# Optimization experiments

Measured on AMD Instinct MI355X. Metric: run time of the kernel, lower is better.

## Reference

```python
import jax, jax.numpy as jnp
import numpy as np

N = 50000      # nodes / stations
E = 600000     # edges
IN = 16        # in_channels
ED = 8         # edge_dim
HID = 128      # hidden
H = 4          # heads
C = HID // H   # 32 per-head channels
EMB = HID // 2 # station embedding dim
FEAT = HID - EMB
SLOPE = 0.2    # GATv2 LeakyReLU negative slope


def setup_inputs() -> dict:
    key = jax.random.key(0)
    ks = jax.random.split(key, 32)
    r = lambda i, shape, s=0.05: (jax.random.normal(ks[i], shape, jnp.float32) * s)
    inp = {
        "x": jax.random.normal(ks[0], (N, IN), jnp.float32),
        "node_idx": jax.random.randint(ks[1], (N,), 0, N),
        "edge_index": jax.random.randint(ks[2], (2, E), 0, N),
        "edge_attr": jax.random.normal(ks[3], (E, ED), jnp.float32),
        # params
        "emb": r(4, (N, EMB)),
        "W_in": r(5, (IN, FEAT)), "b_in": jnp.zeros((FEAT,), jnp.float32),
        # conv1 (GATv2: lin_l, lin_r, lin_edge, att, out bias)
        "Wl1": r(6, (HID, HID)), "bl1": jnp.zeros((HID,), jnp.float32),
        "Wr1": r(7, (HID, HID)), "br1": jnp.zeros((HID,), jnp.float32),
        "We1": r(8, (ED, HID)),  "be1": jnp.zeros((HID,), jnp.float32),
        "att1": r(9, (H, C)),    "bo1": jnp.zeros((HID,), jnp.float32),
        # conv2
        "Wl2": r(10, (HID, HID)), "bl2": jnp.zeros((HID,), jnp.float32),
        "Wr2": r(11, (HID, HID)), "br2": jnp.zeros((HID,), jnp.float32),
        "We2": r(12, (ED, HID)),  "be2": jnp.zeros((HID,), jnp.float32),
        "att2": r(13, (H, C)),    "bo2": jnp.zeros((HID,), jnp.float32),
        # layer norms
        "g1": jnp.ones((HID,), jnp.float32), "beta1": jnp.zeros((HID,), jnp.float32),
        "g2": jnp.ones((HID,), jnp.float32), "beta2": jnp.zeros((HID,), jnp.float32),
        # output head
        "W_out": r(14, (HID, 1)), "b_out": jnp.zeros((1,), jnp.float32),
    }
    return inp


def _gatv2(x, src, dst, ea, Wl, bl, Wr, br, We, be, att, bo):
    # x: [N,HID] -> per-head projections [N,H,C]
    xl = (x @ Wl + bl).reshape(-1, H, C)   # source transform
    xr = (x @ Wr + br).reshape(-1, H, C)   # target transform
    ee = (ea @ We + be).reshape(-1, H, C)  # edge transform [E,H,C]
    s = jax.nn.leaky_relu(xl[src] + xr[dst] + ee, SLOPE)  # [E,H,C]
    logit = jnp.einsum('ehc,hc->eh', s, att)              # [E,H]
    # segment softmax over destination node
    amax = jax.lax.stop_gradient(jax.ops.segment_max(logit, dst, num_segments=N))
    amax = jnp.where(jnp.isfinite(amax), amax, 0.0)
    ex = jnp.exp(logit - amax[dst])
    den = jax.ops.segment_sum(ex, dst, num_segments=N)
    alpha = ex / den[dst]                                  # [E,H]
    out = jax.ops.segment_sum(xl[src] * alpha[..., None], dst, num_segments=N)
    return out.reshape(-1, HID) + bo


def _ln(x, g, b):
    mu = x.mean(-1, keepdims=True)
    v = ((x - mu) ** 2).mean(-1, keepdims=True)
    return (x - mu) * jax.lax.rsqrt(v + 1e-5) * g + b


def reference(x, node_idx, edge_index, edge_attr, emb, W_in, b_in,
              Wl1, bl1, Wr1, br1, We1, be1, att1, bo1,
              Wl2, bl2, Wr2, br2, We2, be2, att2, bo2,
              g1, beta1, g2, beta2, W_out, b_out):
    src, dst = edge_index[0], edge_index[1]
    feat = jax.nn.relu(x @ W_in + b_in)                       # [N,FEAT]
    z = jnp.concatenate([feat, emb[node_idx]], axis=-1)       # [N,HID]
    h = jax.nn.relu(_gatv2(z, src, dst, edge_attr, Wl1, bl1, Wr1, br1, We1, be1, att1, bo1))
    z = _ln(z + h, g1, beta1)
    h = jax.nn.relu(_gatv2(z, src, dst, edge_attr, Wl2, bl2, Wr2, br2, We2, be2, att2, bo2))
    z = _ln(z + h, g2, beta2)
    return (z @ W_out + b_out).squeeze(-1)                    # [N]
```

## Files before the change

### kernel.cpp

```cpp
#include <hip/hip_runtime.h>
#include <hip/hip_bf16.h>

#define NN 50000
#define NE 600000
#define IND 16
#define EDD 8
#define HIDD 128
#define NH 4
#define CC 32
#define EMBD 64
#define FEATD 64
#define NB_SCAN ((NN + 255) / 256)

typedef __hip_bfloat16 bf16;
typedef __attribute__((ext_vector_type(8))) short bshort8;
typedef __attribute__((ext_vector_type(4))) float floatx4;

__device__ __forceinline__ unsigned short f2bu(float f) {
    unsigned int u = __float_as_uint(f);
    u += 0x7fffu + ((u >> 16) & 1u);
    return (unsigned short)(u >> 16);
}

template <bool F32>
__device__ __forceinline__ float LD(const void* p, long long i) {
    if constexpr (F32) return ((const float*)p)[i];
    else return __bfloat162float(((const bf16*)p)[i]);
}

__device__ __forceinline__ bool is_f32(const int* cnt) { return *cnt > 8; }

__global__ void k_detinit(const unsigned short* __restrict__ x, int nhalf,
                          int* __restrict__ cnt, int* __restrict__ deg,
                          int* __restrict__ dcnt) {
    if (blockIdx.x == 0) {
        __shared__ int red[256];
        int hits = 0;
        for (int i = threadIdx.x; i < nhalf; i += 256)
            if ((x[i] & 0x7F80u) == 0x7F80u) hits++;
        red[threadIdx.x] = hits;
        __syncthreads();
        for (int o = 128; o; o >>= 1) {
            if (threadIdx.x < o) red[threadIdx.x] += red[threadIdx.x + o];
            __syncthreads();
        }
        if (threadIdx.x == 0) *cnt = red[0];
    } else {
        int gid = (blockIdx.x - 1) * 256 + threadIdx.x;
        if (gid < NN) deg[gid] = 0;
        if (blockIdx.x == 1 && threadIdx.x < 64) dcnt[threadIdx.x] = 0;
    }
}

__global__ void k_hist(const int* __restrict__ ei, int* __restrict__ deg, int* __restrict__ rank) {
    int e = blockIdx.x * blockDim.x + threadIdx.x;
    if (e < NE) rank[e] = atomicAdd(&deg[ei[NE + e]], 1);
}

__global__ void k_scan1(const int* __restrict__ deg, int* __restrict__ off,
                        int* __restrict__ bsum, int* __restrict__ dcnt,
                        int* __restrict__ rankd) {
    __shared__ int tile[256];
    __shared__ int lh[64];
    __shared__ int lbase[64];
    int t = threadIdx.x;
    int gid = blockIdx.x * 256 + t;
    if (t < 64) lh[t] = 0;
    __syncthreads();
    int v = (gid < NN) ? deg[gid] : 0;
    int b = min(v, 63);
    int lr = 0;
    if (gid < NN) lr = atomicAdd(&lh[b], 1);
    tile[t] = v;
    __syncthreads();
    if (t < 64) lbase[t] = lh[t] ? atomicAdd(&dcnt[t], lh[t]) : 0;
    #pragma unroll
    for (int o = 1; o < 256; o <<= 1) {
        int u = (t >= o) ? tile[t - o] : 0;
        __syncthreads();
        tile[t] += u;
        __syncthreads();
    }
    if (gid < NN) {
        off[gid] = tile[t] - v;
        rankd[gid] = lbase[b] + lr;
    }
    if (t == 255) bsum[blockIdx.x] = tile[255];
}
__global__ void k_scan2(int* __restrict__ bsum, int* __restrict__ dcnt,
                        int* __restrict__ dbase) {
    __shared__ int tile[256];
    __shared__ int d2[64];
    int t = threadIdx.x;
    int v = (t < NB_SCAN) ? bsum[t] : 0;
    tile[t] = v;
    int dv = (t < 64) ? dcnt[t] : 0;
    if (t < 64) d2[t] = dv;
    __syncthreads();
    #pragma unroll
    for (int o = 1; o < 256; o <<= 1) {
        int u = (t >= o) ? tile[t - o] : 0;
        __syncthreads();
        tile[t] += u;
        __syncthreads();
    }
    #pragma unroll
    for (int o = 1; o < 64; o <<= 1) {
        int u = (t >= o && t < 64) ? d2[t - o] : 0;
        __syncthreads();
        if (t < 64) d2[t] += u;
        __syncthreads();
    }
    if (t < NB_SCAN) bsum[t] = tile[t] - v;
    if (t < 64) dbase[t] = d2[t] - dv;
}
__global__ void k_scan3(int* __restrict__ off, const int* __restrict__ bsum,
                        const int* __restrict__ deg, const int* __restrict__ rankd,
                        const int* __restrict__ dbase, int* __restrict__ perm) {
    int gid = blockIdx.x * 256 + threadIdx.x;
    if (gid < NN) {
        off[gid] += bsum[blockIdx.x];
        int b = min(deg[gid], 63);
        perm[dbase[b] + rankd[gid]] = gid;
    }
    if (gid == 0) off[NN] = NE;
}

template <bool F32>
__device__ void fill_impl(const int* __restrict__ ei, const int* __restrict__ off,
                          const int* __restrict__ rank, int* __restrict__ esrc,
                          uint4* __restrict__ ea8, const void* ea) {
    int e = blockIdx.x * blockDim.x + threadIdx.x;
    if (e >= NE) return;
    if (e < 6) {
        esrc[NE + e] = 0;
        uint4 z; z.x = 0; z.y = 0; z.z = 0; z.w = 0;
        ea8[NE + e] = z;
    }
    int slot = off[ei[NE + e]] + rank[e];
    esrc[slot] = ei[e];
    unsigned int w[4];
    #pragma unroll
    for (int d = 0; d < 4; d++) {
        unsigned int lo = f2bu(LD<F32>(ea, (long long)e * EDD + 2 * d));
        unsigned int hi = f2bu(LD<F32>(ea, (long long)e * EDD + 2 * d + 1));
        w[d] = lo | (hi << 16);
    }
    uint4 v; v.x = w[0]; v.y = w[1]; v.z = w[2]; v.w = w[3];
    ea8[slot] = v;
}
__global__ void k_fill(const int* cnt, const int* ei, const int* off, const int* rank,
                       int* esrc, uint4* ea8, const void* ea) {
    if (is_f32(cnt)) fill_impl<true>(ei, off, rank, esrc, ea8, ea);
    else             fill_impl<false>(ei, off, rank, esrc, ea8, ea);
}

template <bool F32>
__device__ void bzpw_impl(const void* x, const int* __restrict__ node_idx, const void* emb,
                          const void* W_in, const void* b_in, bf16* __restrict__ zb,
                          const void* Wl1, const void* bl1, const void* Wr1, const void* br1,
                          const void* Wl2, const void* bl2, const void* Wr2, const void* br2,
                          bf16* __restrict__ wbT, float* __restrict__ bias) {
    int t = threadIdx.x;
    if (blockIdx.x < NN) {
        int n = blockIdx.x;
        float val;
        if (t < FEATD) {
            float acc = LD<F32>(b_in, t);
            #pragma unroll
            for (int k = 0; k < IND; k++)
                acc += LD<F32>(x, (long long)n * IND + k) * LD<F32>(W_in, k * FEATD + t);
            val = fmaxf(acc, 0.f);
        } else {
            val = LD<F32>(emb, (long long)node_idx[n] * EMBD + (t - FEATD));
        }
        zb[n * HIDD + t] = __float2bfloat16(val);
    } else {
        int bid = blockIdx.x - NN;
        int layer = bid >> 8;
        int n = bid & 255;
        const void* W = layer ? (n < HIDD ? Wl2 : Wr2) : (n < HIDD ? Wl1 : Wr1);
        const void* b = layer ? (n < HIDD ? bl2 : br2) : (n < HIDD ? bl1 : br1);
        int nn = n & (HIDD - 1);
        wbT[(layer * 256 + n) * HIDD + t] = __float2bfloat16(LD<F32>(W, t * HIDD + nn));
        if (t == 0) bias[layer * 256 + n] = LD<F32>(b, nn);
    }
}
__global__ void k_bzpw(const int* cnt, const void* x, const int* node_idx, const void* emb,
                       const void* W_in, const void* b_in, bf16* zb,
                       const void* Wl1, const void* bl1, const void* Wr1, const void* br1,
                       const void* Wl2, const void* bl2, const void* Wr2, const void* br2,
                       bf16* wbT, float* bias) {
    if (is_f32(cnt)) bzpw_impl<true>(x, node_idx, emb, W_in, b_in, zb, Wl1, bl1, Wr1, br1,
                                     Wl2, bl2, Wr2, br2, wbT, bias);
    else             bzpw_impl<false>(x, node_idx, emb, W_in, b_in, zb, Wl1, bl1, Wr1, br1,
                                      Wl2, bl2, Wr2, br2, wbT, bias);
}

__global__ __launch_bounds__(256) void k_projmm(const bf16* __restrict__ zb,
                                                const bf16* __restrict__ wbT,
                                                const float* __restrict__ bias,
                                                bf16* __restrict__ xl, bf16* __restrict__ xr) {
    int wave = threadIdx.x >> 6, lane = threadIdx.x & 63;
    int m0 = blockIdx.x * 32;
    int n0 = wave * 64;
    int l15 = lane & 15, q = lane >> 4;
    bshort8 bfr[4][4];
    #pragma unroll
    for (int j = 0; j < 4; j++)
        #pragma unroll
        for (int s = 0; s < 4; s++)
            bfr[j][s] = *(const bshort8*)(wbT + ((n0 + j * 16 + l15) << 7) + s * 32 + q * 8);
    float bv[4];
    #pragma unroll
    for (int j = 0; j < 4; j++) bv[j] = bias[n0 + j * 16 + l15];
    const bf16* arow0 = zb + ((m0 + l15) << 7) + q * 8;
    const bf16* arow1 = arow0 + (16 << 7);
    bshort8 a0[4], a1[4];
    #pragma unroll
    for (int s = 0; s < 4; s++) a0[s] = *(const bshort8*)(arow0 + s * 32);
    #pragma unroll
    for (int s = 0; s < 4; s++) a1[s] = *(const bshort8*)(arow1 + s * 32);
    #pragma unroll
    for (int mi = 0; mi < 2; mi++) {
        floatx4 acc0 = {0.f, 0.f, 0.f, 0.f}, acc1 = acc0, acc2 = acc0, acc3 = acc0;
        #pragma unroll
        for (int s = 0; s < 4; s++) {
            bshort8 a = mi ? a1[s] : a0[s];
            acc0 = __builtin_amdgcn_mfma_f32_16x16x32_bf16(a, bfr[0][s], acc0, 0, 0, 0);
            acc1 = __builtin_amdgcn_mfma_f32_16x16x32_bf16(a, bfr[1][s], acc1, 0, 0, 0);
            acc2 = __builtin_amdgcn_mfma_f32_16x16x32_bf16(a, bfr[2][s], acc2, 0, 0, 0);
            acc3 = __builtin_amdgcn_mfma_f32_16x16x32_bf16(a, bfr[3][s], acc3, 0, 0, 0);
        }
        floatx4 accs[4] = {acc0, acc1, acc2, acc3};
        #pragma unroll
        for (int j = 0; j < 4; j++) {
            int colg = n0 + j * 16 + l15;
            bf16* dst = (colg < HIDD) ? (xl + colg) : (xr + (colg - HIDD));
            #pragma unroll
            for (int r = 0; r < 4; r++) {
                int rowc = m0 + mi * 16 + q * 4 + r;
                if (rowc < NN) dst[rowc << 7] = __float2bfloat16(accs[j][r] + bv[j]);
            }
        }
    }
}

__device__ __forceinline__ void edge_body(uint4 eu, uint2 xu, const float (*wv)[4],
                                          const float* bev, const float* at,
                                          const float* xrv, float mask,
                                          float* acc, float& den) {
    float e[8];
    e[0] = __uint_as_float(eu.x << 16); e[1] = __uint_as_float(eu.x & 0xffff0000u);
    e[2] = __uint_as_float(eu.y << 16); e[3] = __uint_as_float(eu.y & 0xffff0000u);
    e[4] = __uint_as_float(eu.z << 16); e[5] = __uint_as_float(eu.z & 0xffff0000u);
    e[6] = __uint_as_float(eu.w << 16); e[7] = __uint_as_float(eu.w & 0xffff0000u);
    float xv[4];
    xv[0] = __uint_as_float(xu.x << 16); xv[1] = __uint_as_float(xu.x & 0xffff0000u);
    xv[2] = __uint_as_float(xu.y << 16); xv[3] = __uint_as_float(xu.y & 0xffff0000u);
    float ls = 0.f;
    #pragma unroll
    for (int j = 0; j < 4; j++) {
        float ee = bev[j];
        #pragma unroll
        for (int d = 0; d < EDD; d++) ee += e[d] * wv[d][j];
        float s = xv[j] + xrv[j] + ee;
        s = fmaxf(s, 0.2f * s);
        ls += s * at[j];
    }
    ls += __shfl_xor(ls, 1);
    ls += __shfl_xor(ls, 2);
    ls += __shfl_xor(ls, 4);
    float ex = __expf(ls) * mask;
    #pragma unroll
    for (int j = 0; j < 4; j++) acc[j] += ex * xv[j];
    den += ex;
}

template <bool F32, bool LAST>
__device__ void gat_impl(const int* __restrict__ perm,
                         const int* __restrict__ off, const int* __restrict__ esrc,
                         const uint4* __restrict__ ea8,
                         const void* We, const void* be, const void* att,
                         const bf16* __restrict__ xl, const bf16* __restrict__ xr,
                         const void* bo, bf16* __restrict__ zb,
                         const void* g, const void* beta,
                         const void* Wo, const void* bout, void* out) {
    int wave = threadIdx.x >> 6;
    int half = (threadIdx.x >> 5) & 1;
    int lane5 = threadIdx.x & 31;
    int n = perm[blockIdx.x * 8 + wave * 2 + half];
    int c0 = lane5 << 2;
    float wv[EDD][4], at[4], bev[4];
    #pragma unroll
    for (int d = 0; d < EDD; d++)
        #pragma unroll
        for (int j = 0; j < 4; j++) wv[d][j] = LD<F32>(We, d * HIDD + c0 + j);
    #pragma unroll
    for (int j = 0; j < 4; j++) {
        at[j] = LD<F32>(att, c0 + j);
        bev[j] = LD<F32>(be, c0 + j);
    }
    uint2 xru = *(const uint2*)(xr + (n << 7) + c0);
    float xrv[4];
    xrv[0] = __uint_as_float(xru.x << 16);
    xrv[1] = __uint_as_float(xru.x & 0xffff0000u);
    xrv[2] = __uint_as_float(xru.y << 16);
    xrv[3] = __uint_as_float(xru.y & 0xffff0000u);
    int lo = off[n], hi = off[n + 1];
    float accA[4] = {0.f, 0.f, 0.f, 0.f}, accB[4] = {0.f, 0.f, 0.f, 0.f};
    float denA = 0.f, denB = 0.f;
    if (lo < hi) {
        int sA = esrc[lo],      sB = esrc[lo + 1];
        uint4 eA = ea8[lo],     eB = ea8[lo + 1];
        uint2 xA = *(const uint2*)(xl + (sA << 7) + c0);
        uint2 xB = *(const uint2*)(xl + (sB << 7) + c0);
        int snA = esrc[lo + 2], snB = esrc[lo + 3];
        uint4 enA = ea8[lo + 2], enB = ea8[lo + 3];
        for (int i = lo; i < hi; i += 2) {
            uint2 xnA = *(const uint2*)(xl + (snA << 7) + c0);
            uint2 xnB = *(const uint2*)(xl + (snB << 7) + c0);
            int s2A = esrc[i + 4],  s2B = esrc[i + 5];
            uint4 e2A = ea8[i + 4], e2B = ea8[i + 5];
            edge_body(eA, xA, wv, bev, at, xrv, 1.f, accA, denA);
            float mB = (i + 1 < hi) ? 1.f : 0.f;
            edge_body(eB, xB, wv, bev, at, xrv, mB, accB, denB);
            eA = enA; eB = enB; xA = xnA; xB = xnB;
            snA = s2A; snB = s2B; enA = e2A; enB = e2B;
        }
        #pragma unroll
        for (int j = 0; j < 4; j++) accA[j] += accB[j];
        denA += denB;
    }
    float inv = (denA > 0.f) ? 1.0f / denA : 0.f;
    uint2 zu = *(const uint2*)(zb + (n << 7) + c0);
    float zv[4];
    zv[0] = __uint_as_float(zu.x << 16);
    zv[1] = __uint_as_float(zu.x & 0xffff0000u);
    zv[2] = __uint_as_float(zu.y << 16);
    zv[3] = __uint_as_float(zu.y & 0xffff0000u);
    float v[4];
    float s = 0.f;
    #pragma unroll
    for (int j = 0; j < 4; j++) {
        float hv = fmaxf(accA[j] * inv + LD<F32>(bo, c0 + j), 0.f);
        v[j] = zv[j] + hv;
        s += v[j];
    }
    #pragma unroll
    for (int m = 16; m; m >>= 1) s += __shfl_xor(s, m);
    float mu = s * (1.f / HIDD);
    float s2 = 0.f;
    float dv[4];
    #pragma unroll
    for (int j = 0; j < 4; j++) { dv[j] = v[j] - mu; s2 += dv[j] * dv[j]; }
    #pragma unroll
    for (int m = 16; m; m >>= 1) s2 += __shfl_xor(s2, m);
    float rs = rsqrtf(s2 * (1.f / HIDD) + 1e-5f);
    float o[4];
    #pragma unroll
    for (int j = 0; j < 4; j++)
        o[j] = dv[j] * rs * LD<F32>(g, c0 + j) + LD<F32>(beta, c0 + j);
    if constexpr (!LAST) {
        uint2 pk;
        pk.x = (unsigned int)f2bu(o[0]) | ((unsigned int)f2bu(o[1]) << 16);
        pk.y = (unsigned int)f2bu(o[2]) | ((unsigned int)f2bu(o[3]) << 16);
        *(uint2*)(zb + (n << 7) + c0) = pk;
    } else {
        float po = 0.f;
        #pragma unroll
        for (int j = 0; j < 4; j++) po += o[j] * LD<F32>(Wo, c0 + j);
        #pragma unroll
        for (int m = 16; m; m >>= 1) po += __shfl_xor(po, m);
        if (lane5 == 0) {
            float r = po + LD<F32>(bout, 0);
            if constexpr (F32) ((float*)out)[n] = r;
            else               ((bf16*)out)[n] = __float2bfloat16(r);
        }
    }
}
__global__ void k_gat(const int* cnt, const int* perm, const int* off, const int* esrc,
                      const uint4* ea8, const void* We, const void* be, const void* att,
                      const bf16* xl, const bf16* xr, const void* bo, bf16* zb,
                      const void* g, const void* beta) {
    if (is_f32(cnt)) gat_impl<true, false>(perm, off, esrc, ea8, We, be, att, xl, xr, bo, zb, g, beta, nullptr, nullptr, nullptr);
    else             gat_impl<false, false>(perm, off, esrc, ea8, We, be, att, xl, xr, bo, zb, g, beta, nullptr, nullptr, nullptr);
}
__global__ void k_gat_last(const int* cnt, const int* perm, const int* off, const int* esrc,
                           const uint4* ea8, const void* We, const void* be, const void* att,
                           const bf16* xl, const bf16* xr, const void* bo, bf16* zb,
                           const void* g, const void* beta,
                           const void* Wo, const void* bout, void* out) {
    if (is_f32(cnt)) gat_impl<true, true>(perm, off, esrc, ea8, We, be, att, xl, xr, bo, zb, g, beta, Wo, bout, out);
    else             gat_impl<false, true>(perm, off, esrc, ea8, We, be, att, xl, xr, bo, zb, g, beta, Wo, bout, out);
}

extern "C" void kernel_launch(void* const* d_in, const int* in_sizes, int n_in,
                              void* d_out, int out_size, void* d_ws, size_t ws_size,
                              hipStream_t stream) {
    const void* x        = d_in[0];
    const int*  node_idx = (const int*)d_in[1];
    const int*  ei       = (const int*)d_in[2];
    const void* ea       = d_in[3];
    const void* emb      = d_in[4];
    const void* W_in     = d_in[5];
    const void* b_in     = d_in[6];
    const void* Wl1 = d_in[7];  const void* bl1 = d_in[8];
    const void* Wr1 = d_in[9];  const void* br1 = d_in[10];
    const void* We1 = d_in[11]; const void* be1 = d_in[12];
    const void* att1 = d_in[13]; const void* bo1 = d_in[14];
    const void* Wl2 = d_in[15]; const void* bl2 = d_in[16];
    const void* Wr2 = d_in[17]; const void* br2 = d_in[18];
    const void* We2 = d_in[19]; const void* be2 = d_in[20];
    const void* att2 = d_in[21]; const void* bo2 = d_in[22];
    const void* g1 = d_in[23]; const void* beta1 = d_in[24];
    const void* g2 = d_in[25]; const void* beta2 = d_in[26];
    const void* W_out = d_in[27]; const void* b_out = d_in[28];

    int*   cnt   = (int*)d_ws;
    uint4* ea8   = (uint4*)((char*)d_ws + 256);
    bf16*  zb    = (bf16*)(ea8 + NE + 8);
    bf16*  xl    = zb + NN * HIDD;
    bf16*  xr    = xl + NN * HIDD;
    bf16*  wbT   = xr + NN * HIDD;
    float* bias  = (float*)(wbT + 2 * 256 * HIDD);
    int*   off   = (int*)(bias + 512);
    int*   deg   = off + NN + 1;
    int*   rank  = deg + NN;
    int*   rankd = rank + NE;
    int*   perm  = rankd + NN;
    int*   esrc  = perm + NN;
    int*   bsum  = esrc + NE + 8;
    int*   dcnt  = bsum + 256;
    int*   dbase = dcnt + 64;

    int nhalf = in_sizes[0] < 16384 ? in_sizes[0] : 16384;
    k_detinit<<<NB_SCAN + 1, 256, 0, stream>>>((const unsigned short*)x, nhalf, cnt, deg, dcnt);
    k_hist<<<(NE + 255) / 256, 256, 0, stream>>>(ei, deg, rank);
    k_scan1<<<NB_SCAN, 256, 0, stream>>>(deg, off, bsum, dcnt, rankd);
    k_scan2<<<1, 256, 0, stream>>>(bsum, dcnt, dbase);
    k_scan3<<<NB_SCAN, 256, 0, stream>>>(off, bsum, deg, rankd, dbase, perm);
    k_bzpw<<<NN + 512, HIDD, 0, stream>>>(cnt, x, node_idx, emb, W_in, b_in, zb,
                                          Wl1, bl1, Wr1, br1, Wl2, bl2, Wr2, br2, wbT, bias);
    k_fill<<<(NE + 255) / 256, 256, 0, stream>>>(cnt, ei, off, rank, esrc, ea8, ea);

    k_projmm<<<(NN + 31) / 32, 256, 0, stream>>>(zb, wbT, bias, xl, xr);
    k_gat<<<NN / 8, 256, 0, stream>>>(cnt, perm, off, esrc, ea8, We1, be1, att1, xl, xr, bo1, zb, g1, beta1);

    k_projmm<<<(NN + 31) / 32, 256, 0, stream>>>(zb, wbT + 256 * HIDD, bias + 256, xl, xr);
    k_gat_last<<<NN / 8, 256, 0, stream>>>(cnt, perm, off, esrc, ea8, We2, be2, att2, xl, xr, bo2, zb,
                                           g2, beta2, W_out, b_out, d_out);
}
```

Before: 403.1 us.

## Gather edge data via slot-ordered edge ids and merge prep kernels

The CSR fill now happens in two steps. The scan kernel scatters only edge ids into their slots. The prep kernel then reads in slot order, so esrc and the bf16 edge attributes are written coalesced rather than scattered, at the cost of gathered reads of ei and ea. The node-embedding build and weight transpose are merged into that same prep launch, with 256-thread blocks covering two rows each, which cuts one kernel launch. In the GAT kernels the per-node xr term is folded into the edge bias ahead of the edge loop, removing one add per edge channel.

```diff
diff --git a/kernel.cpp b/kernel.cpp
--- a/kernel.cpp
+++ b/kernel.cpp
@@ -11,6 +11,8 @@
 #define EMBD 64
 #define FEATD 64
 #define NB_SCAN ((NN + 255) / 256)
+#define NB_EDGE ((NE + 255) / 256)
+#define NB_SLOT ((NE + 6 + 255) / 256)
 
 typedef __hip_bfloat16 bf16;
 typedef __attribute__((ext_vector_type(8))) short bshort8;
@@ -114,87 +116,94 @@
     if (t < NB_SCAN) bsum[t] = tile[t] - v;
     if (t < 64) dbase[t] = d2[t] - dv;
 }
-__global__ void k_scan3(int* __restrict__ off, const int* __restrict__ bsum,
-                        const int* __restrict__ deg, const int* __restrict__ rankd,
-                        const int* __restrict__ dbase, int* __restrict__ perm) {
-    int gid = blockIdx.x * 256 + threadIdx.x;
-    if (gid < NN) {
-        off[gid] += bsum[blockIdx.x];
-        int b = min(deg[gid], 63);
-        perm[dbase[b] + rankd[gid]] = gid;
-    }
-    if (gid == 0) off[NN] = NE;
+__global__ void k_scan3x(const int* __restrict__ off, const int* __restrict__ bsum,
+                         const int* __restrict__ deg, const int* __restrict__ rankd,
+                         const int* __restrict__ dbase, int* __restrict__ perm,
+                         int* __restrict__ offF, const int* __restrict__ ei,
+                         const int* __restrict__ rank, int* __restrict__ eid) {
+    if (blockIdx.x < NB_SCAN) {
+        int gid = blockIdx.x * 256 + threadIdx.x;
+        if (gid < NN) {
+            offF[gid] = off[gid] + bsum[blockIdx.x];
+            int b = min(deg[gid], 63);
+            perm[dbase[b] + rankd[gid]] = gid;
+        }
+        if (gid == 0) offF[NN] = NE;
+    } else {
+        int e = (blockIdx.x - NB_SCAN) * 256 + threadIdx.x;
+        if (e < NE) {
+            int dst = ei[NE + e];
+            int slot = off[dst] + bsum[dst >> 8] + rank[e];
+            eid[slot] = e;
+        }
+    }
 }
 
 template <bool F32>
-__device__ void fill_impl(const int* __restrict__ ei, const int* __restrict__ off,
-                          const int* __restrict__ rank, int* __restrict__ esrc,
-                          uint4* __restrict__ ea8, const void* ea) {
-    int e = blockIdx.x * blockDim.x + threadIdx.x;
-    if (e >= NE) return;
-    if (e < 6) {
-        esrc[NE + e] = 0;
-        uint4 z; z.x = 0; z.y = 0; z.z = 0; z.w = 0;
-        ea8[NE + e] = z;
-    }
-    int slot = off[ei[NE + e]] + rank[e];
-    esrc[slot] = ei[e];
-    unsigned int w[4];
-    #pragma unroll
-    for (int d = 0; d < 4; d++) {
-        unsigned int lo = f2bu(LD<F32>(ea, (long long)e * EDD + 2 * d));
-        unsigned int hi = f2bu(LD<F32>(ea, (long long)e * EDD + 2 * d + 1));
-        w[d] = lo | (hi << 16);
-    }
-    uint4 v; v.x = w[0]; v.y = w[1]; v.z = w[2]; v.w = w[3];
-    ea8[slot] = v;
-}
-__global__ void k_fill(const int* cnt, const int* ei, const int* off, const int* rank,
-                       int* esrc, uint4* ea8, const void* ea) {
-    if (is_f32(cnt)) fill_impl<true>(ei, off, rank, esrc, ea8, ea);
-    else             fill_impl<false>(ei, off, rank, esrc, ea8, ea);
-}
-
-template <bool F32>
-__device__ void bzpw_impl(const void* x, const int* __restrict__ node_idx, const void* emb,
+__device__ void prep_impl(const int* __restrict__ eid, const int* __restrict__ ei,
+                          const void* ea, int* __restrict__ esrc, uint4* __restrict__ ea8,
+                          const void* x, const int* __restrict__ node_idx, const void* emb,
                           const void* W_in, const void* b_in, bf16* __restrict__ zb,
                           const void* Wl1, const void* bl1, const void* Wr1, const void* br1,
                           const void* Wl2, const void* bl2, const void* Wr2, const void* br2,
                           bf16* __restrict__ wbT, float* __restrict__ bias) {
     int t = threadIdx.x;
-    if (blockIdx.x < NN) {
-        int n = blockIdx.x;
+    if (blockIdx.x < NB_SLOT) {
+        int s = blockIdx.x * 256 + t;
+        if (s < NE) {
+            int e = eid[s];
+            esrc[s] = ei[e];
+            unsigned int w[4];
+            #pragma unroll
+            for (int d = 0; d < 4; d++) {
+                unsigned int lo = f2bu(LD<F32>(ea, (long long)e * EDD + 2 * d));
+                unsigned int hi = f2bu(LD<F32>(ea, (long long)e * EDD + 2 * d + 1));
+                w[d] = lo | (hi << 16);
+            }
+            uint4 v; v.x = w[0]; v.y = w[1]; v.z = w[2]; v.w = w[3];
+            ea8[s] = v;
+        } else if (s < NE + 6) {
+            esrc[s] = 0;
+            uint4 z; z.x = 0; z.y = 0; z.z = 0; z.w = 0;
+            ea8[s] = z;
+        }
+    } else if (blockIdx.x < NB_SLOT + NN / 2) {
+        int bid = blockIdx.x - NB_SLOT;
+        int n = bid * 2 + (t >> 7);
+        int tt = t & 127;
         float val;
-        if (t < FEATD) {
-            float acc = LD<F32>(b_in, t);
+        if (tt < FEATD) {
+            float acc = LD<F32>(b_in, tt);
             #pragma unroll
             for (int k = 0; k < IND; k++)
-                acc += LD<F32>(x, (long long)n * IND + k) * LD<F32>(W_in, k * FEATD + t);
+                acc += LD<F32>(x, (long long)n * IND + k) * LD<F32>(W_in, k * FEATD + tt);
             val = fmaxf(acc, 0.f);
         } else {
-            val = LD<F32>(emb, (long long)node_idx[n] * EMBD + (t - FEATD));
-        }
-        zb[n * HIDD + t] = __float2bfloat16(val);
+            val = LD<F32>(emb, (long long)node_idx[n] * EMBD + (tt - FEATD));
+        }
+        zb[n * HIDD + tt] = __float2bfloat16(val);
     } else {
-        int bid = blockIdx.x - NN;
-        int layer = bid >> 8;
-        int n = bid & 255;
+        int wid = (blockIdx.x - NB_SLOT - NN / 2) * 2 + (t >> 7);
+        int layer = wid >> 8;
+        int n = wid & 255;
+        int tt = t & 127;
         const void* W = layer ? (n < HIDD ? Wl2 : Wr2) : (n < HIDD ? Wl1 : Wr1);
         const void* b = layer ? (n < HIDD ? bl2 : br2) : (n < HIDD ? bl1 : br1);
         int nn = n & (HIDD - 1);
-        wbT[(layer * 256 + n) * HIDD + t] = __float2bfloat16(LD<F32>(W, t * HIDD + nn));
-        if (t == 0) bias[layer * 256 + n] = LD<F32>(b, nn);
-    }
-}
-__global__ void k_bzpw(const int* cnt, const void* x, const int* node_idx, const void* emb,
-                       const void* W_in, const void* b_in, bf16* zb,
+        wbT[(layer * 256 + n) * HIDD + tt] = __float2bfloat16(LD<F32>(W, tt * HIDD + nn));
+        if (tt == 0) bias[layer * 256 + n] = LD<F32>(b, nn);
+    }
+}
+__global__ void k_prep(const int* cnt, const int* eid, const int* ei, const void* ea,
+                       int* esrc, uint4* ea8, const void* x, const int* node_idx,
+                       const void* emb, const void* W_in, const void* b_in, bf16* zb,
                        const void* Wl1, const void* bl1, const void* Wr1, const void* br1,
                        const void* Wl2, const void* bl2, const void* Wr2, const void* br2,
                        bf16* wbT, float* bias) {
-    if (is_f32(cnt)) bzpw_impl<true>(x, node_idx, emb, W_in, b_in, zb, Wl1, bl1, Wr1, br1,
-                                     Wl2, bl2, Wr2, br2, wbT, bias);
-    else             bzpw_impl<false>(x, node_idx, emb, W_in, b_in, zb, Wl1, bl1, Wr1, br1,
-                                      Wl2, bl2, Wr2, br2, wbT, bias);
+    if (is_f32(cnt)) prep_impl<true>(eid, ei, ea, esrc, ea8, x, node_idx, emb, W_in, b_in, zb,
+                                     Wl1, bl1, Wr1, br1, Wl2, bl2, Wr2, br2, wbT, bias);
+    else             prep_impl<false>(eid, ei, ea, esrc, ea8, x, node_idx, emb, W_in, b_in, zb,
+                                      Wl1, bl1, Wr1, br1, Wl2, bl2, Wr2, br2, wbT, bias);
 }
 
 __global__ __launch_bounds__(256) void k_projmm(const bf16* __restrict__ zb,
@@ -247,8 +256,7 @@
 }
 
 __device__ __forceinline__ void edge_body(uint4 eu, uint2 xu, const float (*wv)[4],
-                                          const float* bev, const float* at,
-                                          const float* xrv, float mask,
+                                          const float* base, const float* at, float mask,
                                           float* acc, float& den) {
     float e[8];
     e[0] = __uint_as_float(eu.x << 16); e[1] = __uint_as_float(eu.x & 0xffff0000u);
@@ -261,10 +269,10 @@
     float ls = 0.f;
     #pragma unroll
     for (int j = 0; j < 4; j++) {
-        float ee = bev[j];
+        float ee = base[j];
         #pragma unroll
         for (int d = 0; d < EDD; d++) ee += e[d] * wv[d][j];
-        float s = xv[j] + xrv[j] + ee;
+        float s = xv[j] + ee;
         s = fmaxf(s, 0.2f * s);
         ls += s * at[j];
     }
@@ -291,22 +299,22 @@
     int lane5 = threadIdx.x & 31;
     int n = perm[blockIdx.x * 8 + wave * 2 + half];
     int c0 = lane5 << 2;
-    float wv[EDD][4], at[4], bev[4];
+    float wv[EDD][4], at[4], base[4];
     #pragma unroll
     for (int d = 0; d < EDD; d++)
         #pragma unroll
         for (int j = 0; j < 4; j++) wv[d][j] = LD<F32>(We, d * HIDD + c0 + j);
-    #pragma unroll
-    for (int j = 0; j < 4; j++) {
-        at[j] = LD<F32>(att, c0 + j);
-        bev[j] = LD<F32>(be, c0 + j);
-    }
     uint2 xru = *(const uint2*)(xr + (n << 7) + c0);
     float xrv[4];
     xrv[0] = __uint_as_float(xru.x << 16);
     xrv[1] = __uint_as_float(xru.x & 0xffff0000u);
     xrv[2] = __uint_as_float(xru.y << 16);
     xrv[3] = __uint_as_float(xru.y & 0xffff0000u);
+    #pragma unroll
+    for (int j = 0; j < 4; j++) {
+        at[j] = LD<F32>(att, c0 + j);
+        base[j] = LD<F32>(be, c0 + j) + xrv[j];
+    }
     int lo = off[n], hi = off[n + 1];
     float accA[4] = {0.f, 0.f, 0.f, 0.f}, accB[4] = {0.f, 0.f, 0.f, 0.f};
     float denA = 0.f, denB = 0.f;
@@ -322,9 +330,9 @@
             uint2 xnB = *(const uint2*)(xl + (snB << 7) + c0);
             int s2A = esrc[i + 4],  s2B = esrc[i + 5];
             uint4 e2A = ea8[i + 4], e2B = ea8[i + 5];
-            edge_body(eA, xA, wv, bev, at, xrv, 1.f, accA, denA);
+            edge_body(eA, xA, wv, base, at, 1.f, accA, denA);
             float mB = (i + 1 < hi) ? 1.f : 0.f;
-            edge_body(eB, xB, wv, bev, at, xrv, mB, accB, denB);
+            edge_body(eB, xB, wv, base, at, mB, accB, denB);
             eA = enA; eB = enB; xA = xnA; xB = xnB;
             snA = s2A; snB = s2B; enA = e2A; enB = e2B;
         }
@@ -425,29 +433,33 @@
     bf16*  wbT   = xr + NN * HIDD;
     float* bias  = (float*)(wbT + 2 * 256 * HIDD);
     int*   off   = (int*)(bias + 512);
-    int*   deg   = off + NN + 1;
+    int*   offF  = off + NN;
+    int*   deg   = offF + NN + 1;
     int*   rank  = deg + NN;
     int*   rankd = rank + NE;
     int*   perm  = rankd + NN;
-    int*   esrc  = perm + NN;
+    int*   eid   = perm + NN;
+    int*   esrc  = eid + NE + 8;
     int*   bsum  = esrc + NE + 8;
     int*   dcnt  = bsum + 256;
     int*   dbase = dcnt + 64;
 
     int nhalf = in_sizes[0] < 16384 ? in_sizes[0] : 16384;
     k_detinit<<<NB_SCAN + 1, 256, 0, stream>>>((const unsigned short*)x, nhalf, cnt, deg, dcnt);
-    k_hist<<<(NE + 255) / 256, 256, 0, stream>>>(ei, deg, rank);
+    k_hist<<<NB_EDGE, 256, 0, stream>>>(ei, deg, rank);
     k_scan1<<<NB_SCAN, 256, 0, stream>>>(deg, off, bsum, dcnt, rankd);
     k_scan2<<<1, 256, 0, stream>>>(bsum, dcnt, dbase);
-    k_scan3<<<NB_SCAN, 256, 0, stream>>>(off, bsum, deg, rankd, dbase, perm);
-    k_bzpw<<<NN + 512, HIDD, 0, stream>>>(cnt, x, node_idx, emb, W_in, b_in, zb,
-                                          Wl1, bl1, Wr1, br1, Wl2, bl2, Wr2, br2, wbT, bias);
-    k_fill<<<(NE + 255) / 256, 256, 0, stream>>>(cnt, ei, off, rank, esrc, ea8, ea);
+    k_scan3x<<<NB_SCAN + NB_EDGE, 256, 0, stream>>>(off, bsum, deg, rankd, dbase, perm,
+                                                    offF, ei, rank, eid);
+    k_prep<<<NB_SLOT + NN / 2 + 256, 256, 0, stream>>>(cnt, eid, ei, ea, esrc, ea8,
+                                                       x, node_idx, emb, W_in, b_in, zb,
+                                                       Wl1, bl1, Wr1, br1, Wl2, bl2, Wr2, br2,
+                                                       wbT, bias);
 
     k_projmm<<<(NN + 31) / 32, 256, 0, stream>>>(zb, wbT, bias, xl, xr);
-    k_gat<<<NN / 8, 256, 0, stream>>>(cnt, perm, off, esrc, ea8, We1, be1, att1, xl, xr, bo1, zb, g1, beta1);
+    k_gat<<<NN / 8, 256, 0, stream>>>(cnt, perm, offF, esrc, ea8, We1, be1, att1, xl, xr, bo1, zb, g1, beta1);
 
     k_projmm<<<(NN + 31) / 32, 256, 0, stream>>>(zb, wbT + 256 * HIDD, bias + 256, xl, xr);
-    k_gat_last<<<NN / 8, 256, 0, stream>>>(cnt, perm, off, esrc, ea8, We2, be2, att2, xl, xr, bo2, zb,
+    k_gat_last<<<NN / 8, 256, 0, stream>>>(cnt, perm, offF, esrc, ea8, We2, be2, att2, xl, xr, bo2, zb,
                                            g2, beta2, W_out, b_out, d_out);
 }
```

After: 423.0 us. 4.9% more time.
